# Performance work log

Measured on AMD Instinct MI355X. Metric: run time of the kernel, lower is better.

The kernel has to match this reference:

```python
import jax, jax.numpy as jnp
import numpy as np
import math

IN, HID, OUT = 256, 512, 256
B, T = 256, 256

def setup_inputs() -> dict:
    key = jax.random.key(0)
    ks = jax.random.split(key, 20)
    stdv = 1.0 / math.sqrt(HID)
    u = lambda k, shape: jax.random.uniform(k, shape, jnp.float32, -stdv, stdv)
    inp = {
        "x": jax.random.normal(ks[0], (B, T, IN), jnp.float32),
        "c": jax.random.normal(ks[1], (B, T, IN), jnp.float32),
        "h0": jax.random.uniform(ks[2], (B, HID), jnp.float32),
        "w_xr": u(ks[3], (IN, HID)), "w_hr": u(ks[4], (HID, HID)), "w_cr": u(ks[5], (IN, HID)),
        "w_xz": u(ks[6], (IN, HID)), "w_hz": u(ks[7], (HID, HID)), "w_cz": u(ks[8], (IN, HID)),
        "w_xh": u(ks[9], (IN, HID)), "w_hh": u(ks[10], (HID, HID)), "w_ch": u(ks[11], (IN, HID)),
        "b_r": u(ks[12], (HID,)), "b_z": u(ks[13], (HID,)), "b_h": u(ks[14], (HID,)),
        "w_out": u(ks[15], (HID, OUT)), "b_out": u(ks[16], (OUT,)),
    }
    return inp

def reference(x, c, h0, w_xr, w_hr, w_cr, w_xz, w_hz, w_cz, w_xh, w_hh, w_ch,
              b_r, b_z, b_h, w_out, b_out):
    # Precompute the input/context projections for ALL timesteps as 3 big GEMMs
    # (math identical to the per-step mm's in the original).
    pre_z = jnp.einsum('bti,ih->bth', x, w_xz) + jnp.einsum('bti,ih->bth', c, w_cz) + b_z
    pre_r = jnp.einsum('bti,ih->bth', x, w_xr) + jnp.einsum('bti,ih->bth', c, w_cr) + b_r
    pre_h = jnp.einsum('bti,ih->bth', x, w_xh) + jnp.einsum('bti,ih->bth', c, w_ch) + b_h

    def step(h, pres):
        pz, pr, ph = pres  # each [B, HID]
        z = jax.nn.sigmoid(pz + h @ w_hz)
        r = jax.nn.sigmoid(pr + h @ w_hr)
        h_tilde = jnp.tanh(ph + (r * h) @ w_hh)
        h_new = (1.0 - z) * h + z * h_tilde
        return h_new, h_new

    # scan over time: move time axis to leading
    pres = (pre_z.transpose(1, 0, 2), pre_r.transpose(1, 0, 2), pre_h.transpose(1, 0, 2))
    h_last, hs_t = jax.lax.scan(step, h0, pres)
    hs = hs_t.transpose(1, 0, 2)  # [B, T, HID]
    output = jax.nn.relu(h_last @ w_out + b_out)  # relu(relu(.)) == relu(.)
    return output, hs
```

## Files before the change

### kernel.cpp

```cpp
#include <hip/hip_runtime.h>
#include <stdint.h>
#include <stdio.h>

typedef unsigned short ushort_t;
typedef float   f32x4  __attribute__((ext_vector_type(4)));
typedef short   bf16x8 __attribute__((ext_vector_type(8)));

#define B_    256
#define T_    256
#define IN_   256
#define HID_  512

#define CTR_WORDS 8448
#define OFF_CTR   0
#define OFF_BT    33792
#define OFF_WT    1606656
#define OFF_HB    3179520
#define OFF_UB    3441664
#define OFF_PRE   3703808
#define WS_NEED   205030400ULL

static __device__ __forceinline__ unsigned short f2bf(float f) {
  union { float f; unsigned u; } v; v.f = f;
  unsigned r = v.u + 0x7FFFu + ((v.u >> 16) & 1u);
  return (unsigned short)(r >> 16);
}
static __device__ __forceinline__ float bf2f(unsigned short h) {
  union { unsigned u; float f; } v; v.u = ((unsigned)h) << 16; return v.f;
}
static __device__ __forceinline__ float sigm(float x) {
  float e = exp2f(-1.4426950408889634f * x);
  return __builtin_amdgcn_rcpf(1.0f + e);
}
static __device__ __forceinline__ float tanh_f(float x) {
  float e = exp2f(2.8853900817779268f * x);
  return 1.0f - 2.0f * __builtin_amdgcn_rcpf(e + 1.0f);
}

static __device__ __forceinline__ void st_b16_dev(void* p, unsigned v) {
  asm volatile("global_store_short %0, %1, off sc0 sc1" :: "v"(p), "v"(v) : "memory");
}
static __device__ __forceinline__ void ld4_b128_dev(const void* p0, const void* p1,
                                                    const void* p2, const void* p3,
                                                    f32x4& a, f32x4& b, f32x4& c, f32x4& d) {
  asm volatile("global_load_dwordx4 %0, %4, off sc0 sc1\n\t"
               "global_load_dwordx4 %1, %5, off sc0 sc1\n\t"
               "global_load_dwordx4 %2, %6, off sc0 sc1\n\t"
               "global_load_dwordx4 %3, %7, off sc0 sc1\n\t"
               "s_waitcnt vmcnt(0)"
               : "=&v"(a), "=&v"(b), "=&v"(c), "=&v"(d)
               : "v"(p0), "v"(p1), "v"(p2), "v"(p3)
               : "memory");
}

__global__ void __launch_bounds__(256) k_prep(
    const float* __restrict__ wxz, const float* __restrict__ wxr, const float* __restrict__ wxh,
    const float* __restrict__ wcz, const float* __restrict__ wcr, const float* __restrict__ wch,
    const float* __restrict__ whz, const float* __restrict__ whr, const float* __restrict__ whh,
    unsigned* __restrict__ ctr, ushort_t* __restrict__ bt, ushort_t* __restrict__ wT)
{
  int e = blockIdx.x * 256 + threadIdx.x;
  if (e < CTR_WORDS) ctr[e] = 0u;

  {
    int n = e >> 9, k = e & 511;
    int g = n >> 9, j = n & 511;
    const float* wx = (g == 0) ? wxz : (g == 1) ? wxr : wxh;
    const float* wc = (g == 0) ? wcz : (g == 1) ? wcr : wch;
    float v = (k < 256) ? wx[k * 512 + j] : wc[(k - 256) * 512 + j];
    bt[e] = f2bf(v);
  }
  {
    int g = e >> 18, rem = e & 262143;
    int j = rem >> 9, k = rem & 511;
    const float* wh = (g == 0) ? whz : (g == 1) ? whr : whh;
    wT[g * 262144 + j * 512 + (k ^ ((j & 7) << 3))] = f2bf(wh[k * 512 + j]);
  }
}

__global__ void __launch_bounds__(256) k_pregemm(
    const float* __restrict__ x, const float* __restrict__ c,
    const ushort_t* __restrict__ bt,
    const float* __restrict__ b_z, const float* __restrict__ b_r, const float* __restrict__ b_h,
    ushort_t* __restrict__ pre)
{
  __shared__ ushort_t As[128 * 64];
  __shared__ ushort_t Bs[128 * 64];
  int blk = blockIdx.x;
  int bm = blk % 512, bn = blk / 512;
  int tid = threadIdx.x, lane = tid & 63, wv = tid >> 6;
  int wm = (wv >> 1) * 64, wn = (wv & 1) * 64;
  int cl = lane & 15, rg = lane >> 4;
  f32x4 acc[4][4] = {};

  for (int kt = 0; kt < 8; ++kt) {
    int k0 = kt * 64;
    const float* srcA = (k0 < 256) ? x : c;
    int kbase = (k0 < 256) ? k0 : (k0 - 256);
    #pragma unroll
    for (int i = 0; i < 4; ++i) {
      int ch = tid + 256 * i;
      int m = ch >> 3, k8 = ch & 7;
      const float* p = srcA + (size_t)(bm * 128 + m) * 256 + kbase + k8 * 8;
      float4 f0 = *(const float4*)p;
      float4 f1 = *(const float4*)(p + 4);
      bf16x8 v;
      v[0]=(short)f2bf(f0.x); v[1]=(short)f2bf(f0.y); v[2]=(short)f2bf(f0.z); v[3]=(short)f2bf(f0.w);
      v[4]=(short)f2bf(f1.x); v[5]=(short)f2bf(f1.y); v[6]=(short)f2bf(f1.z); v[7]=(short)f2bf(f1.w);
      *(bf16x8*)((char*)As + ((m * 128 + k8 * 16) ^ ((m & 7) << 4))) = v;
    }
    #pragma unroll
    for (int i = 0; i < 4; ++i) {
      int ch = tid + 256 * i;
      int n = ch >> 3, k8 = ch & 7;
      int k8s = k8 ^ (n & 7);
      bf16x8 v = *(const bf16x8*)(bt + (size_t)(bn * 128 + n) * 512 + k0 + k8s * 8);
      *(bf16x8*)((char*)Bs + (n * 128 + k8 * 16)) = v;
    }
    __syncthreads();
    #pragma unroll
    for (int kk = 0; kk < 2; ++kk) {
      bf16x8 af[4], bfr[4];
      int kb = kk * 32 + rg * 8;
      #pragma unroll
      for (int fm = 0; fm < 4; ++fm) {
        int m = wm + fm * 16 + cl;
        af[fm] = *(const bf16x8*)((char*)As + (((m * 64 + kb) * 2) ^ ((m & 7) << 4)));
      }
      #pragma unroll
      for (int fn = 0; fn < 4; ++fn) {
        int n = wn + fn * 16 + cl;
        bfr[fn] = *(const bf16x8*)((char*)Bs + (((n * 64 + kb) * 2) ^ ((n & 7) << 4)));
      }
      #pragma unroll
      for (int fm = 0; fm < 4; ++fm)
        #pragma unroll
        for (int fn = 0; fn < 4; ++fn)
          acc[fm][fn] = __builtin_amdgcn_mfma_f32_16x16x32_bf16(af[fm], bfr[fn], acc[fm][fn], 0, 0, 0);
    }
    __syncthreads();
  }
  #pragma unroll
  for (int fm = 0; fm < 4; ++fm)
    #pragma unroll
    for (int fn = 0; fn < 4; ++fn) {
      int ng = bn * 128 + wn + fn * 16 + cl;
      int g = ng >> 9, j = ng & 511;
      const float* bias = (g == 0) ? b_z : (g == 1) ? b_r : b_h;
      float bv = bias[j];
      #pragma unroll
      for (int i = 0; i < 4; ++i) {
        int M = bm * 128 + wm + fm * 16 + rg * 4 + i;
        int b = M >> 8, t = M & 255;
        pre[(((size_t)g * 256 + t) * 256 + b) * 512 + j] = f2bf(acc[fm][fn][i] + bv);
      }
    }
}

struct ScanArgs {
  const ushort_t* wT;
  const ushort_t* pre;
  ushort_t* hbuf;
  ushort_t* ubuf;
  unsigned* ctr;
  const float* h0;
  float* hs;
};
#define SMEM_SCAN 133120

static __device__ __forceinline__ void xchg_read_swz(const ushort_t* __restrict__ src,
                                                     ushort_t* dst, int tid) {
  const void* p[4];
  f32x4 v0, v1, v2, v3;
  #pragma unroll
  for (int i = 0; i < 4; ++i) { int ch = tid + 256 * i; p[i] = src + (size_t)ch * 8; }
  ld4_b128_dev(p[0], p[1], p[2], p[3], v0, v1, v2, v3);
  f32x4 vv[4] = { v0, v1, v2, v3 };
  #pragma unroll
  for (int i = 0; i < 4; ++i) {
    int ch = tid + 256 * i;
    int row = ch >> 6, k8 = ch & 63;
    *(f32x4*)((char*)dst + (((row * 512 + k8 * 8) * 2) ^ ((row & 7) << 4))) = vv[i];
  }
}

static __device__ __forceinline__ void fill_init(const float* __restrict__ src,
                                                 ushort_t* hA, float* hsl, int J, int tid) {
  #pragma unroll
  for (int i = 0; i < 4; ++i) {
    int ch = tid + 256 * i;
    int row = ch >> 6, k8 = ch & 63;
    const float* p = src + (size_t)row * 512 + k8 * 8;
    float4 f0 = *(const float4*)p;
    float4 f1 = *(const float4*)(p + 4);
    bf16x8 v;
    v[0]=(short)f2bf(f0.x); v[1]=(short)f2bf(f0.y); v[2]=(short)f2bf(f0.z); v[3]=(short)f2bf(f0.w);
    v[4]=(short)f2bf(f1.x); v[5]=(short)f2bf(f1.y); v[6]=(short)f2bf(f1.z); v[7]=(short)f2bf(f1.w);
    *(bf16x8*)((char*)hA + (((row * 512 + k8 * 8) * 2) ^ ((row & 7) << 4))) = v;
    int kb = k8 * 8;
    if (kb >= J && kb < J + 32) {
      float* q = hsl + row * 32 + (kb - J);
      q[0]=f0.x; q[1]=f0.y; q[2]=f0.z; q[3]=f0.w; q[4]=f1.x; q[5]=f1.y; q[6]=f1.z; q[7]=f1.w;
    }
  }
}

static __device__ __forceinline__ void signal_wait(unsigned* c, unsigned* abortf, bool& dead) {
  if (dead) return;
  __hip_atomic_fetch_add(c, 1u, __ATOMIC_RELAXED, __HIP_MEMORY_SCOPE_AGENT);
  unsigned it = 0;
  while (__hip_atomic_load(c, __ATOMIC_RELAXED, __HIP_MEMORY_SCOPE_AGENT) < 16u) {
    if (((++it) & 63u) == 0u) {
      if (it > (1u << 18)) { __hip_atomic_store(abortf, 1u, __ATOMIC_RELAXED, __HIP_MEMORY_SCOPE_AGENT); dead = true; break; }
      if (__hip_atomic_load(abortf, __ATOMIC_RELAXED, __HIP_MEMORY_SCOPE_AGENT) != 0u) { dead = true; break; }
    }
  }
}

__global__ void __launch_bounds__(256, 1) k_scan(ScanArgs A) {
  extern __shared__ char smem[];
  ushort_t* Wt  = (ushort_t*)smem;
  ushort_t* hA  = (ushort_t*)(smem + 98304);
  ushort_t* uA  = (ushort_t*)(smem + 114688);
  float*    hsl = (float*)(smem + 131072);

  int blk = blockIdx.x;
  int g = blk & 15, wgj = blk >> 4;
  int J = wgj * 32;
  int b0 = g * 16;
  int tid = threadIdx.x, lane = tid & 63, wv = tid >> 6;
  int cl = lane & 15, rg = lane >> 4;
  unsigned* ctrU = A.ctr + (g * 2 + 0) * 256;
  unsigned* ctrH = A.ctr + (g * 2 + 1) * 256;
  unsigned* abortf = A.ctr + 16 * 2 * 256;
  bool dead = false;

  #pragma unroll
  for (int gt = 0; gt < 3; ++gt) {
    const ushort_t* src = A.wT + gt * 262144 + J * 512;
    ushort_t* dst = Wt + gt * 16384;
    #pragma unroll
    for (int i = 0; i < 8; ++i) {
      int ch = tid + 256 * i;
      *(bf16x8*)(dst + ch * 8) = *(const bf16x8*)(src + ch * 8);
    }
  }
  fill_init(A.h0 + (size_t)b0 * 512, hA, hsl, J, tid);
  __syncthreads();

  #pragma unroll 1
  for (int t = 0; t < 256; ++t) {
    float pg[4], ph[4];
    {
      int gate1 = wv >> 1;
      int col = J + (wv & 1) * 16 + cl;
      const ushort_t* pp  = A.pre + (((size_t)gate1 * 256 + t) * 256 + b0) * 512;
      const ushort_t* pph = A.pre + (((size_t)2 * 256 + t) * 256 + b0) * 512;
      #pragma unroll
      for (int i = 0; i < 4; ++i) {
        int row = rg * 4 + i;
        pg[i] = bf2f(pp[(size_t)row * 512 + col]);
        ph[i] = (wv < 2) ? bf2f(pph[(size_t)row * 512 + col]) : 0.0f;
      }
    }
    int gate = wv >> 1;
    int jl = (wv & 1) * 16 + cl;
    f32x4 acc = {};
    #pragma unroll
    for (int kk = 0; kk < 16; ++kk) {
      int kb = kk * 32 + rg * 8;
      bf16x8 av = *(const bf16x8*)((char*)hA + (((cl * 512 + kb) * 2) ^ ((cl & 7) << 4)));
      bf16x8 bv = *(const bf16x8*)((char*)Wt + gate * 32768 + (((jl * 512 + kb) * 2) ^ ((jl & 7) << 4)));
      acc = __builtin_amdgcn_mfma_f32_16x16x32_bf16(av, bv, acc, 0, 0, 0);
    }
    float zv[4] = {0.f, 0.f, 0.f, 0.f};
    if (wv < 2) {
      #pragma unroll
      for (int i = 0; i < 4; ++i) zv[i] = sigm(acc[i] + pg[i]);
    } else {
      #pragma unroll
      for (int i = 0; i < 4; ++i) {
        float r = sigm(acc[i] + pg[i]);
        int row = rg * 4 + i;
        float u = r * hsl[row * 32 + jl];
        st_b16_dev(A.ubuf + (size_t)(b0 + row) * 512 + J + jl, (unsigned)f2bf(u));
      }
    }
    asm volatile("s_waitcnt vmcnt(0)" ::: "memory");
    __syncthreads();
    if (tid == 0) signal_wait(ctrU + t, abortf, dead);
    __syncthreads();
    xchg_read_swz(A.ubuf + (size_t)b0 * 512, uA, tid);
    __syncthreads();
    if (wv < 2) {
      f32x4 acc2 = {};
      int jl2 = wv * 16 + cl;
      #pragma unroll
      for (int kk = 0; kk < 16; ++kk) {
        int kb = kk * 32 + rg * 8;
        bf16x8 av = *(const bf16x8*)((char*)uA + (((cl * 512 + kb) * 2) ^ ((cl & 7) << 4)));
        bf16x8 bv = *(const bf16x8*)((char*)Wt + 2 * 32768 + (((jl2 * 512 + kb) * 2) ^ ((jl2 & 7) << 4)));
        acc2 = __builtin_amdgcn_mfma_f32_16x16x32_bf16(av, bv, acc2, 0, 0, 0);
      }
      #pragma unroll
      for (int i = 0; i < 4; ++i) {
        int row = rg * 4 + i;
        float th = tanh_f(acc2[i] + ph[i]);
        float hv = hsl[row * 32 + jl2];
        float hn = hv + zv[i] * (th - hv);
        hsl[row * 32 + jl2] = hn;
        int b = b0 + row;
        st_b16_dev(A.hbuf + (size_t)b * 512 + J + jl2, (unsigned)f2bf(hn));
        A.hs[((size_t)b * 256 + t) * 512 + J + jl2] = hn;
      }
    }
    asm volatile("s_waitcnt vmcnt(0)" ::: "memory");
    __syncthreads();
    if (tid == 0) signal_wait(ctrH + t, abortf, dead);
    __syncthreads();
    xchg_read_swz(A.hbuf + (size_t)b0 * 512, hA, tid);
    __syncthreads();
  }
}

__global__ void __launch_bounds__(256) k_out(const float* __restrict__ hs,
                                             const float* __restrict__ w_out,
                                             const float* __restrict__ b_out,
                                             float* __restrict__ out) {
  __shared__ float hl[512];
  int b = blockIdx.x, o = threadIdx.x;
  const float* hrow = hs + ((size_t)b * 256 + 255) * 512;
  for (int i = threadIdx.x; i < 512; i += 256) hl[i] = hrow[i];
  __syncthreads();
  float acc = b_out[o];
  #pragma unroll 8
  for (int k = 0; k < 512; ++k) acc += hl[k] * w_out[k * 256 + o];
  out[(size_t)b * 256 + o] = fmaxf(acc, 0.0f);
}

extern "C" void kernel_launch(void* const* d_in, const int* in_sizes, int n_in,
                              void* d_out, int out_size, void* d_ws, size_t ws_size,
                              hipStream_t stream) {
  const float* x    = (const float*)d_in[0];
  const float* c    = (const float*)d_in[1];
  const float* h0   = (const float*)d_in[2];
  const float* wxr  = (const float*)d_in[3];
  const float* whr  = (const float*)d_in[4];
  const float* wcr  = (const float*)d_in[5];
  const float* wxz  = (const float*)d_in[6];
  const float* whz  = (const float*)d_in[7];
  const float* wcz  = (const float*)d_in[8];
  const float* wxh  = (const float*)d_in[9];
  const float* whh  = (const float*)d_in[10];
  const float* wch  = (const float*)d_in[11];
  const float* br   = (const float*)d_in[12];
  const float* bz   = (const float*)d_in[13];
  const float* bh   = (const float*)d_in[14];
  const float* wout = (const float*)d_in[15];
  const float* bout = (const float*)d_in[16];

  char* ws = (char*)d_ws;
  unsigned*  ctr  = (unsigned*)(ws + OFF_CTR);
  ushort_t*  bt   = (ushort_t*)(ws + OFF_BT);
  ushort_t*  wT   = (ushort_t*)(ws + OFF_WT);
  ushort_t*  hbuf = (ushort_t*)(ws + OFF_HB);
  ushort_t*  ubuf = (ushort_t*)(ws + OFF_UB);
  ushort_t*  pre  = (ushort_t*)(ws + OFF_PRE);
  float* out = (float*)d_out;
  float* hs  = out + 65536;

  if (ws_size < WS_NEED)
    fprintf(stderr, "[kernel] WARNING ws_size=%zu < needed %llu\n", ws_size, WS_NEED);

  k_prep<<<3072, 256, 0, stream>>>(wxz, wxr, wxh, wcz, wcr, wch, whz, whr, whh, ctr, bt, wT);
  k_pregemm<<<6144, 256, 0, stream>>>(x, c, bt, bz, br, bh, pre);

  hipFuncSetAttribute((const void*)k_scan, hipFuncAttributeMaxDynamicSharedMemorySize, SMEM_SCAN);
  ScanArgs sa{wT, pre, hbuf, ubuf, ctr, h0, hs};
  void* args[] = { &sa };
  hipError_t e = hipLaunchCooperativeKernel(k_scan, dim3(256), dim3(256), args,
                                            (unsigned)SMEM_SCAN, stream);
  if (e != hipSuccess)
    fprintf(stderr, "[kernel] coop launch failed: %d (%s)\n", (int)e, hipGetErrorString(e));

  k_out<<<256, 256, 0, stream>>>(hs, wout, bout, out);
}
```

Measured before the change: 1.979 ms.

## Remap scan workgroups by XCD and use monotonic L2-atomic group barriers

Each scan workgroup reads its hardware XCD id and the blocks are regrouped so that each 16-block batch group sits on one XCD where possible. For such pure groups a single monotonic counter is polled with L2-scope atomics by every wave, replacing the per-timestep counters spun on by thread 0 alone; mixed groups fall back to device-scope polling. It also prefetches the next step's pre-activations during the barrier, splits MFMA accumulation into two chains, and moves the hs global store after the exchange. This is meant to cut cross-XCD synchronization latency on the serial critical path, at the cost of a startup grid-wide rendezvous and a more fragile barrier protocol.

```diff
diff --git a/kernel.cpp b/kernel.cpp
--- a/kernel.cpp
+++ b/kernel.cpp
@@ -11,7 +11,7 @@
 #define IN_   256
 #define HID_  512
 
-#define CTR_WORDS 8448
+#define CTR_WORDS 4096
 #define OFF_CTR   0
 #define OFF_BT    33792
 #define OFF_WT    1606656
@@ -39,6 +39,21 @@
 
 static __device__ __forceinline__ void st_b16_dev(void* p, unsigned v) {
   asm volatile("global_store_short %0, %1, off sc0 sc1" :: "v"(p), "v"(v) : "memory");
+}
+static __device__ __forceinline__ void st_u32_dev(void* p, unsigned v) {
+  asm volatile("global_store_dword %0, %1, off sc0 sc1" :: "v"(p), "v"(v) : "memory");
+}
+static __device__ __forceinline__ unsigned ld_u32_dev(const void* p) {
+  unsigned v;
+  asm volatile("global_load_dword %0, %1, off sc0 sc1\n\ts_waitcnt vmcnt(0)"
+               : "=v"(v) : "v"(p) : "memory");
+  return v;
+}
+static __device__ __forceinline__ unsigned at_add_ret_l2(void* p, unsigned d) {
+  unsigned v;
+  asm volatile("global_atomic_add %0, %1, %2, off sc0\n\ts_waitcnt vmcnt(0)"
+               : "=&v"(v) : "v"(p), "v"(d) : "memory");
+  return v;
 }
 static __device__ __forceinline__ void ld4_b128_dev(const void* p0, const void* p1,
                                                     const void* p2, const void* p3,
@@ -166,7 +181,7 @@
   const float* h0;
   float* hs;
 };
-#define SMEM_SCAN 133120
+#define SMEM_SCAN 134400
 
 static __device__ __forceinline__ void xchg_read_swz(const ushort_t* __restrict__ src,
                                                      ushort_t* dst, int tid) {
@@ -205,35 +220,88 @@
   }
 }
 
-static __device__ __forceinline__ void signal_wait(unsigned* c, unsigned* abortf, bool& dead) {
-  if (dead) return;
-  __hip_atomic_fetch_add(c, 1u, __ATOMIC_RELAXED, __HIP_MEMORY_SCOPE_AGENT);
-  unsigned it = 0;
-  while (__hip_atomic_load(c, __ATOMIC_RELAXED, __HIP_MEMORY_SCOPE_AGENT) < 16u) {
-    if (((++it) & 63u) == 0u) {
-      if (it > (1u << 18)) { __hip_atomic_store(abortf, 1u, __ATOMIC_RELAXED, __HIP_MEMORY_SCOPE_AGENT); dead = true; break; }
-      if (__hip_atomic_load(abortf, __ATOMIC_RELAXED, __HIP_MEMORY_SCOPE_AGENT) != 0u) { dead = true; break; }
-    }
-  }
-}
-
 __global__ void __launch_bounds__(256, 1) k_scan(ScanArgs A) {
   extern __shared__ char smem[];
   ushort_t* Wt  = (ushort_t*)smem;
   ushort_t* hA  = (ushort_t*)(smem + 98304);
   ushort_t* uA  = (ushort_t*)(smem + 114688);
   float*    hsl = (float*)(smem + 131072);
+  unsigned* xcds = (unsigned*)(smem + 133120);
+  volatile int* meta = (int*)(smem + 134208);
 
   int blk = blockIdx.x;
-  int g = blk & 15, wgj = blk >> 4;
-  int J = wgj * 32;
-  int b0 = g * 16;
   int tid = threadIdx.x, lane = tid & 63, wv = tid >> 6;
   int cl = lane & 15, rg = lane >> 4;
-  unsigned* ctrU = A.ctr + (g * 2 + 0) * 256;
-  unsigned* ctrH = A.ctr + (g * 2 + 1) * 256;
-  unsigned* abortf = A.ctr + 16 * 2 * 256;
+  unsigned* abortf = A.ctr + 2080;
+  unsigned* startc = A.ctr + 2112;
+  unsigned* idtab  = A.ctr + 2144;
   bool dead = false;
+
+  if (tid == 0) {
+    unsigned x = __builtin_amdgcn_s_getreg(6164);
+    st_u32_dev(idtab + blk, x);
+    asm volatile("s_waitcnt vmcnt(0)" ::: "memory");
+    __hip_atomic_fetch_add(startc, 1u, __ATOMIC_RELAXED, __HIP_MEMORY_SCOPE_AGENT);
+  }
+  {
+    unsigned it = 0;
+    for (;;) {
+      if (ld_u32_dev(startc) >= 256u) break;
+      if ((((++it) & 1023u) == 0u) && it >= (1u << 20)) {
+        if (tid == 0) st_u32_dev(abortf, 1u);
+        dead = true; break;
+      }
+    }
+  }
+  xcds[tid] = ld_u32_dev(idtab + tid);
+  __syncthreads();
+  if (tid == 0) {
+    unsigned mex = xcds[blk];
+    int less = 0, eqless = 0, eqtot = 0;
+    for (int b = 0; b < 256; ++b) {
+      unsigned v = xcds[b];
+      if (v < mex) less++;
+      else if (v == mex) { eqtot++; if (b < blk) eqless++; }
+    }
+    int idx = less + eqless;
+    int g = idx >> 4;
+    int pure = (g * 16 >= less) && (g * 16 + 16 <= less + eqtot) && (eqtot <= 48);
+    meta[0] = g; meta[1] = idx & 15; meta[2] = pure;
+  }
+  __syncthreads();
+  int g = meta[0];
+  int mIdx = meta[1];
+  int J = mIdx * 32;
+  int b0 = g * 16;
+  bool pure = meta[2] != 0;
+  unsigned* ctrU_P = A.ctr + (g * 2 + 0) * 32;
+  unsigned* ctrH_P = A.ctr + (g * 2 + 1) * 32;
+  unsigned* ctrU_F = A.ctr + 1024 + (g * 2 + 0) * 32;
+  unsigned* ctrH_F = A.ctr + 1024 + (g * 2 + 1) * 32;
+
+  if (pure) {
+    unsigned* pfc = A.ctr + 2432 + g * 32;
+    unsigned* vot = A.ctr + 2944 + g * 32;
+    unsigned* pfb = A.ctr + 3456 + g * 32;
+    if (tid == 0) {
+      unsigned cnt = at_add_ret_l2(pfc, 1u) + 1u;
+      unsigned it = 0;
+      while (cnt < 16u && (++it) < 16384u) cnt = at_add_ret_l2(pfc, 0u);
+      if (cnt >= 16u) {
+        __hip_atomic_fetch_add(vot, 1u, __ATOMIC_RELAXED, __HIP_MEMORY_SCOPE_AGENT);
+        asm volatile("s_waitcnt vmcnt(0)" ::: "memory");
+      }
+      __hip_atomic_fetch_add(pfb, 1u, __ATOMIC_RELAXED, __HIP_MEMORY_SCOPE_AGENT);
+      it = 0;
+      for (;;) {
+        if (ld_u32_dev(pfb) >= 16u) break;
+        if ((++it) >= (1u << 18)) { st_u32_dev(abortf, 1u); dead = true; break; }
+      }
+      meta[2] = (!dead && ld_u32_dev(vot) >= 16u) ? 1 : 0;
+    }
+    __syncthreads();
+    pure = meta[2] != 0;
+  }
 
   #pragma unroll
   for (int gt = 0; gt < 3; ++gt) {
@@ -248,79 +316,136 @@
   fill_init(A.h0 + (size_t)b0 * 512, hA, hsl, J, tid);
   __syncthreads();
 
+  #define GBAR(cwP, cwF, target) do {                                            \
+    __syncthreads();                                                             \
+    if (!dead) {                                                                 \
+      unsigned it = 0;                                                           \
+      if (pure) {                                                                \
+        unsigned r0 = 0;                                                         \
+        if (lane == 0) r0 = at_add_ret_l2((cwP), (wv == 0) ? 1u : 0u) + ((wv == 0) ? 1u : 0u); \
+        unsigned cnt = __builtin_amdgcn_readfirstlane(r0);                       \
+        while (cnt < (target)) {                                                 \
+          if (lane == 0) r0 = at_add_ret_l2((cwP), 0u);                          \
+          cnt = __builtin_amdgcn_readfirstlane(r0);                              \
+          if (((++it) & 63u) == 0u) {                                            \
+            unsigned ab = 0;                                                     \
+            if (lane == 0) {                                                     \
+              if (it >= 65536u) { st_u32_dev(abortf, 1u); ab = 1u; }             \
+              else ab = ld_u32_dev(abortf);                                      \
+            }                                                                    \
+            if (__builtin_amdgcn_readfirstlane(ab) != 0u) { dead = true; break; }\
+          }                                                                      \
+        }                                                                        \
+      } else {                                                                   \
+        if (tid == 0) __hip_atomic_fetch_add((cwF), 1u, __ATOMIC_RELAXED, __HIP_MEMORY_SCOPE_AGENT); \
+        for (;;) {                                                               \
+          unsigned cnt = ld_u32_dev(cwF);                                        \
+          if (cnt >= (target)) break;                                            \
+          if (((++it) & 255u) == 0u) {                                           \
+            if (it >= (1u << 15)) { if (tid == 0) st_u32_dev(abortf, 1u); dead = true; break; } \
+            if (ld_u32_dev(abortf) != 0u) { dead = true; break; }                \
+          }                                                                      \
+        }                                                                        \
+      }                                                                          \
+    }                                                                            \
+  } while (0)
+
+  #define LOAD_PRE(tt, pgu_, phu_) do {                                          \
+    int gate1 = wv >> 1;                                                         \
+    int col = J + (wv & 1) * 16 + cl;                                            \
+    const ushort_t* pp  = A.pre + (((size_t)gate1 * 256 + (tt)) * 256 + b0) * 512; \
+    const ushort_t* pph = A.pre + (((size_t)2 * 256 + (tt)) * 256 + b0) * 512;   \
+    _Pragma("unroll")                                                            \
+    for (int i = 0; i < 4; ++i) {                                                \
+      int row = rg * 4 + i;                                                      \
+      pgu_[i] = pp[(size_t)row * 512 + col];                                     \
+      phu_[i] = (wv < 2) ? pph[(size_t)row * 512 + col] : (ushort_t)0;           \
+    }                                                                            \
+  } while (0)
+
+  ushort_t pgu[4], phu[4];
+  LOAD_PRE(0, pgu, phu);
+
   #pragma unroll 1
   for (int t = 0; t < 256; ++t) {
-    float pg[4], ph[4];
-    {
-      int gate1 = wv >> 1;
-      int col = J + (wv & 1) * 16 + cl;
-      const ushort_t* pp  = A.pre + (((size_t)gate1 * 256 + t) * 256 + b0) * 512;
-      const ushort_t* pph = A.pre + (((size_t)2 * 256 + t) * 256 + b0) * 512;
-      #pragma unroll
-      for (int i = 0; i < 4; ++i) {
-        int row = rg * 4 + i;
-        pg[i] = bf2f(pp[(size_t)row * 512 + col]);
-        ph[i] = (wv < 2) ? bf2f(pph[(size_t)row * 512 + col]) : 0.0f;
-      }
-    }
+    unsigned tgt = (unsigned)(t + 1) << 4;
     int gate = wv >> 1;
     int jl = (wv & 1) * 16 + cl;
-    f32x4 acc = {};
-    #pragma unroll
-    for (int kk = 0; kk < 16; ++kk) {
-      int kb = kk * 32 + rg * 8;
-      bf16x8 av = *(const bf16x8*)((char*)hA + (((cl * 512 + kb) * 2) ^ ((cl & 7) << 4)));
-      bf16x8 bv = *(const bf16x8*)((char*)Wt + gate * 32768 + (((jl * 512 + kb) * 2) ^ ((jl & 7) << 4)));
-      acc = __builtin_amdgcn_mfma_f32_16x16x32_bf16(av, bv, acc, 0, 0, 0);
+    f32x4 aca = {}, acb = {};
+    #pragma unroll
+    for (int kk = 0; kk < 8; ++kk) {
+      int kb0 = (kk * 2) * 32 + rg * 8;
+      int kb1 = (kk * 2 + 1) * 32 + rg * 8;
+      bf16x8 av0 = *(const bf16x8*)((char*)hA + (((cl * 512 + kb0) * 2) ^ ((cl & 7) << 4)));
+      bf16x8 bv0 = *(const bf16x8*)((char*)Wt + gate * 32768 + (((jl * 512 + kb0) * 2) ^ ((jl & 7) << 4)));
+      aca = __builtin_amdgcn_mfma_f32_16x16x32_bf16(av0, bv0, aca, 0, 0, 0);
+      bf16x8 av1 = *(const bf16x8*)((char*)hA + (((cl * 512 + kb1) * 2) ^ ((cl & 7) << 4)));
+      bf16x8 bv1 = *(const bf16x8*)((char*)Wt + gate * 32768 + (((jl * 512 + kb1) * 2) ^ ((jl & 7) << 4)));
+      acb = __builtin_amdgcn_mfma_f32_16x16x32_bf16(av1, bv1, acb, 0, 0, 0);
     }
     float zv[4] = {0.f, 0.f, 0.f, 0.f};
     if (wv < 2) {
       #pragma unroll
-      for (int i = 0; i < 4; ++i) zv[i] = sigm(acc[i] + pg[i]);
+      for (int i = 0; i < 4; ++i) zv[i] = sigm(aca[i] + acb[i] + bf2f(pgu[i]));
     } else {
       #pragma unroll
       for (int i = 0; i < 4; ++i) {
-        float r = sigm(acc[i] + pg[i]);
+        float r = sigm(aca[i] + acb[i] + bf2f(pgu[i]));
         int row = rg * 4 + i;
         float u = r * hsl[row * 32 + jl];
         st_b16_dev(A.ubuf + (size_t)(b0 + row) * 512 + J + jl, (unsigned)f2bf(u));
       }
     }
     asm volatile("s_waitcnt vmcnt(0)" ::: "memory");
+    GBAR(ctrU_P, ctrU_F, tgt);
+    xchg_read_swz(A.ubuf + (size_t)b0 * 512, uA, tid);
+    ushort_t pgu2[4], phu2[4];
+    {
+      int tn = (t < 255) ? (t + 1) : 255;
+      LOAD_PRE(tn, pgu2, phu2);
+    }
     __syncthreads();
-    if (tid == 0) signal_wait(ctrU + t, abortf, dead);
-    __syncthreads();
-    xchg_read_swz(A.ubuf + (size_t)b0 * 512, uA, tid);
-    __syncthreads();
+    float hn[4];
+    int jl2 = wv * 16 + cl;
     if (wv < 2) {
-      f32x4 acc2 = {};
-      int jl2 = wv * 16 + cl;
-      #pragma unroll
-      for (int kk = 0; kk < 16; ++kk) {
-        int kb = kk * 32 + rg * 8;
-        bf16x8 av = *(const bf16x8*)((char*)uA + (((cl * 512 + kb) * 2) ^ ((cl & 7) << 4)));
-        bf16x8 bv = *(const bf16x8*)((char*)Wt + 2 * 32768 + (((jl2 * 512 + kb) * 2) ^ ((jl2 & 7) << 4)));
-        acc2 = __builtin_amdgcn_mfma_f32_16x16x32_bf16(av, bv, acc2, 0, 0, 0);
+      f32x4 a2 = {}, b2 = {};
+      #pragma unroll
+      for (int kk = 0; kk < 8; ++kk) {
+        int kb0 = (kk * 2) * 32 + rg * 8;
+        int kb1 = (kk * 2 + 1) * 32 + rg * 8;
+        bf16x8 av0 = *(const bf16x8*)((char*)uA + (((cl * 512 + kb0) * 2) ^ ((cl & 7) << 4)));
+        bf16x8 bv0 = *(const bf16x8*)((char*)Wt + 2 * 32768 + (((jl2 * 512 + kb0) * 2) ^ ((jl2 & 7) << 4)));
+        a2 = __builtin_amdgcn_mfma_f32_16x16x32_bf16(av0, bv0, a2, 0, 0, 0);
+        bf16x8 av1 = *(const bf16x8*)((char*)uA + (((cl * 512 + kb1) * 2) ^ ((cl & 7) << 4)));
+        bf16x8 bv1 = *(const bf16x8*)((char*)Wt + 2 * 32768 + (((jl2 * 512 + kb1) * 2) ^ ((jl2 & 7) << 4)));
+        b2 = __builtin_amdgcn_mfma_f32_16x16x32_bf16(av1, bv1, b2, 0, 0, 0);
       }
       #pragma unroll
       for (int i = 0; i < 4; ++i) {
         int row = rg * 4 + i;
-        float th = tanh_f(acc2[i] + ph[i]);
+        float th = tanh_f(a2[i] + b2[i] + bf2f(phu[i]));
         float hv = hsl[row * 32 + jl2];
-        float hn = hv + zv[i] * (th - hv);
-        hsl[row * 32 + jl2] = hn;
-        int b = b0 + row;
-        st_b16_dev(A.hbuf + (size_t)b * 512 + J + jl2, (unsigned)f2bf(hn));
-        A.hs[((size_t)b * 256 + t) * 512 + J + jl2] = hn;
+        hn[i] = hv + zv[i] * (th - hv);
+        hsl[row * 32 + jl2] = hn[i];
+        st_b16_dev(A.hbuf + (size_t)(b0 + row) * 512 + J + jl2, (unsigned)f2bf(hn[i]));
       }
     }
     asm volatile("s_waitcnt vmcnt(0)" ::: "memory");
+    GBAR(ctrH_P, ctrH_F, tgt);
+    xchg_read_swz(A.hbuf + (size_t)b0 * 512, hA, tid);
+    if (wv < 2) {
+      #pragma unroll
+      for (int i = 0; i < 4; ++i) {
+        int b = b0 + rg * 4 + i;
+        A.hs[((size_t)b * 256 + t) * 512 + J + jl2] = hn[i];
+      }
+    }
+    #pragma unroll
+    for (int i = 0; i < 4; ++i) { pgu[i] = pgu2[i]; phu[i] = phu2[i]; }
     __syncthreads();
-    if (tid == 0) signal_wait(ctrH + t, abortf, dead);
-    __syncthreads();
-    xchg_read_swz(A.hbuf + (size_t)b0 * 512, hA, tid);
-    __syncthreads();
-  }
+  }
+  #undef GBAR
+  #undef LOAD_PRE
 }
 
 __global__ void __launch_bounds__(256) k_out(const float* __restrict__ hs,
```

Result: slower. 2.473 ms (+24.9%).
